# Performance work log

Measured on AMD Instinct MI355X. Metric: run time of the kernel, lower is better.

Reference implementation:

```python
import jax, jax.numpy as jnp
import numpy as np

B, D, O = 131072, 128, 256

def setup_inputs() -> dict:
    key = jax.random.key(0)
    k1, k2, k3 = jax.random.split(key, 3)
    x = jax.random.normal(k1, (B, D), dtype=jnp.float32)
    weight = jax.random.normal(k2, (O, D), dtype=jnp.float32)
    bias = jax.random.normal(k3, (O,), dtype=jnp.float32)
    return {"x": x, "weight": weight, "bias": bias}

def reference(x, weight, bias):
    # Original: (x[:,None,:] * W[None,:,:]).sum(-1) == linear contraction over D.
    z = jnp.einsum('bd,od->bo', x, weight) + bias  # [B, O]
    # hyperoperation_order == 2 -> elementwise square; activation is None.
    return z * z
```

## Files before the change

kernel.cpp:

```cpp
#include <hip/hip_runtime.h>
#include <hip/hip_bf16.h>


#define B_ROWS 131072
#define D_DIM  128
#define O_DIM  256
#define THREADS 256
#define NBLOCKS 2048
#define ROWS_PER_BLOCK 64
#define TILES (ROWS_PER_BLOCK / 16)

using bf16x8 = __attribute__((ext_vector_type(8))) short;
using f32x4  = __attribute__((ext_vector_type(4))) float;

__device__ __forceinline__ short bf16rne(float f) {
    unsigned u = __builtin_bit_cast(unsigned, f);
    u += 0x7FFFu + ((u >> 16) & 1u);
    return (short)(u >> 16);
}

__device__ __forceinline__ bf16x8 pack8(float4 h0, float4 h1) {
    bf16x8 t;
    t[0] = bf16rne(h0.x); t[1] = bf16rne(h0.y);
    t[2] = bf16rne(h0.z); t[3] = bf16rne(h0.w);
    t[4] = bf16rne(h1.x); t[5] = bf16rne(h1.y);
    t[6] = bf16rne(h1.z); t[7] = bf16rne(h1.w);
    return t;
}

__global__ __launch_bounds__(THREADS, 3)
void hyper_linear_sq_kernel(const float* __restrict__ x,
                            const float* __restrict__ weight,
                            const float* __restrict__ bias,
                            float* __restrict__ out) {
    const int lane  = threadIdx.x & 63;
    const int wid   = threadIdx.x >> 6;
    const int n16   = lane & 15;
    const int quad  = lane >> 4;
    const int cbase = wid * 64;

    bf16x8 bfrag[4][4];
    #pragma unroll
    for (int ct = 0; ct < 4; ++ct) {
        const float* wr = weight + (cbase + ct * 16 + n16) * D_DIM + quad * 8;
        #pragma unroll
        for (int ks = 0; ks < 4; ++ks) {
            float4 h0 = *(const float4*)(wr + ks * 32);
            float4 h1 = *(const float4*)(wr + ks * 32 + 4);
            bfrag[ct][ks] = pack8(h0, h1);
        }
    }

    float bv[4];
    #pragma unroll
    for (int ct = 0; ct < 4; ++ct) bv[ct] = bias[cbase + ct * 16 + n16];

    const int rowbase0 = blockIdx.x * ROWS_PER_BLOCK;

    for (int t = 0; t < TILES; ++t) {
        const int rowbase = rowbase0 + t * 16;

        const float* xr = x + (rowbase + n16) * D_DIM + quad * 8;
        bf16x8 a[4];
        #pragma unroll
        for (int ks = 0; ks < 4; ++ks) {
            float4 h0 = *(const float4*)(xr + ks * 32);
            float4 h1 = *(const float4*)(xr + ks * 32 + 4);
            a[ks] = pack8(h0, h1);
        }

        f32x4 acc[4];
        #pragma unroll
        for (int ct = 0; ct < 4; ++ct) acc[ct] = (f32x4){0.f, 0.f, 0.f, 0.f};

        #pragma unroll
        for (int ks = 0; ks < 4; ++ks) {
            #pragma unroll
            for (int ct = 0; ct < 4; ++ct) {
                acc[ct] = __builtin_amdgcn_mfma_f32_16x16x32_bf16(a[ks], bfrag[ct][ks], acc[ct], 0, 0, 0);
            }
        }

        #pragma unroll
        for (int ct = 0; ct < 4; ++ct) {
            const int col = cbase + ct * 16 + n16;
            #pragma unroll
            for (int r = 0; r < 4; ++r) {
                const int row = rowbase + quad * 4 + r;
                float z = acc[ct][r] + bv[ct];
                out[row * O_DIM + col] = z * z;
            }
        }
    }
}

extern "C" void kernel_launch(void* const* d_in, const int* in_sizes, int n_in,
                              void* d_out, int out_size, void* d_ws, size_t ws_size,
                              hipStream_t stream) {
    const float* x    = (const float*)d_in[0];
    const float* w    = (const float*)d_in[1];
    const float* bias = (const float*)d_in[2];
    float* out        = (float*)d_out;
    hipLaunchKernelGGL(hyper_linear_sq_kernel, dim3(NBLOCKS), dim3(THREADS), 0, stream,
                       x, w, bias, out);
}
```

Measured before the change: 229.6 us.

## Prefetch next x tile and stage outputs through LDS for vector nontemporal stores

Loads the next 16-row x tile into registers while the current tile's MFMAs run. The output is transposed through a per-wave LDS buffer so each lane writes 16-byte vectors with nontemporal stores, replacing scattered 4-byte stores. The goal is to hide global load latency and make the dominant output write traffic coalesced. In exchange it adds LDS traffic and register pressure from the prefetch buffer, and there is no sync between the LDS writes and reads (they are within one wave).

```diff
diff --git a/kernel.cpp b/kernel.cpp
--- a/kernel.cpp
+++ b/kernel.cpp
@@ -7,8 +7,9 @@
 #define O_DIM  256
 #define THREADS 256
 #define NBLOCKS 2048
-#define ROWS_PER_BLOCK 64
-#define TILES (ROWS_PER_BLOCK / 16)
+#define TILES 4
+#define ROWS_PER_BLOCK (TILES * 16)
+#define LDS_PITCH 68
 
 using bf16x8 = __attribute__((ext_vector_type(8))) short;
 using f32x4  = __attribute__((ext_vector_type(4))) float;
@@ -33,6 +34,8 @@
                             const float* __restrict__ weight,
                             const float* __restrict__ bias,
                             float* __restrict__ out) {
+    __shared__ float lds[4][16][LDS_PITCH];
+
     const int lane  = threadIdx.x & 63;
     const int wid   = threadIdx.x >> 6;
     const int n16   = lane & 15;
@@ -56,17 +59,29 @@
     for (int ct = 0; ct < 4; ++ct) bv[ct] = bias[cbase + ct * 16 + n16];
 
     const int rowbase0 = blockIdx.x * ROWS_PER_BLOCK;
+    const float* xbase = x + ((long)rowbase0 + n16) * D_DIM + quad * 8;
 
+    float4 raw[8];
+    #pragma unroll
+    for (int ks = 0; ks < 4; ++ks) {
+        raw[2 * ks]     = *(const float4*)(xbase + ks * 32);
+        raw[2 * ks + 1] = *(const float4*)(xbase + ks * 32 + 4);
+    }
+
+    #pragma unroll
     for (int t = 0; t < TILES; ++t) {
-        const int rowbase = rowbase0 + t * 16;
-
-        const float* xr = x + (rowbase + n16) * D_DIM + quad * 8;
         bf16x8 a[4];
         #pragma unroll
-        for (int ks = 0; ks < 4; ++ks) {
-            float4 h0 = *(const float4*)(xr + ks * 32);
-            float4 h1 = *(const float4*)(xr + ks * 32 + 4);
-            a[ks] = pack8(h0, h1);
+        for (int ks = 0; ks < 4; ++ks) a[ks] = pack8(raw[2 * ks], raw[2 * ks + 1]);
+
+        float4 rawn[8];
+        if (t + 1 < TILES) {
+            const float* xn = xbase + (long)(t + 1) * 16 * D_DIM;
+            #pragma unroll
+            for (int ks = 0; ks < 4; ++ks) {
+                rawn[2 * ks]     = *(const float4*)(xn + ks * 32);
+                rawn[2 * ks + 1] = *(const float4*)(xn + ks * 32 + 4);
+            }
         }
 
         f32x4 acc[4];
@@ -83,13 +98,22 @@
 
         #pragma unroll
         for (int ct = 0; ct < 4; ++ct) {
-            const int col = cbase + ct * 16 + n16;
             #pragma unroll
             for (int r = 0; r < 4; ++r) {
-                const int row = rowbase + quad * 4 + r;
                 float z = acc[ct][r] + bv[ct];
-                out[row * O_DIM + col] = z * z;
+                lds[wid][quad * 4 + r][ct * 16 + n16] = z * z;
             }
+        }
+        #pragma unroll
+        for (int s = 0; s < 4; ++s) {
+            f32x4 v = *(const f32x4*)&lds[wid][s * 4 + quad][n16 * 4];
+            long row = rowbase0 + t * 16 + s * 4 + quad;
+            __builtin_nontemporal_store(v, (f32x4*)(out + row * O_DIM + cbase + n16 * 4));
+        }
+
+        if (t + 1 < TILES) {
+            #pragma unroll
+            for (int i = 0; i < 8; ++i) raw[i] = rawn[i];
         }
     }
 }
```

New measurement: 225.4 us. No clear change (-1.8%).
